# Optimization experiments

Measured on AMD Instinct MI355X. Metric: run time of the kernel, lower is better.

The kernel has to match this reference:

```python
import jax, jax.numpy as jnp
import numpy as np
import math

DIMS = 128
S = 2                     # scalar_attention_num
VS = 0.25                 # voxel_size
QS = 0.01                 # quant_size
L = int((2 * VS + 0.0001) // QS)   # 50, quant table length
GRID = int(2 / VS)        # 8
G = GRID ** 3             # 512 voxel groups
K = 32                    # points per voxel (regularized)
B = 2
N = G * K                 # 16384 points per cloud


def setup_inputs() -> dict:
    key = jax.random.key(0)
    ks = jax.random.split(key, 12)
    inputs = jax.random.normal(ks[0], (B, N, DIMS), jnp.float32)
    # coordinates scaled so per-voxel pairwise distances lie in (-VS, VS)
    coordinates = jax.random.uniform(ks[1], (B, N, 3), jnp.float32) * VS
    # groups: partition of the N points into G voxels of K points each
    groups = jnp.tile(jnp.arange(N, dtype=jnp.int32).reshape(1, G, K), (B, 1, 1))
    effective_groups = jnp.tile(jnp.arange(G, dtype=jnp.int32)[None], (B, 1))
    qkv_w = jax.random.normal(ks[2], (S, DIMS, 3 * DIMS), jnp.float32) * 0.02
    qkv_b = jnp.zeros((S, 3 * DIMS), jnp.float32)
    table_x = jax.random.normal(ks[3], (S, 3, L, DIMS), jnp.float32) * 0.02
    table_y = jax.random.normal(ks[4], (S, 3, L, DIMS), jnp.float32) * 0.02
    table_z = jax.random.normal(ks[5], (S, 3, L, DIMS), jnp.float32) * 0.02
    trans_w = jax.random.normal(ks[6], (DIMS * (S + 1), DIMS), jnp.float32) * 0.02
    trans_b = jnp.zeros((DIMS,), jnp.float32)
    ln_g = jnp.ones((DIMS,), jnp.float32)
    ln_b = jnp.zeros((DIMS,), jnp.float32)
    return {"inputs": inputs, "coordinates": coordinates, "qkv_w": qkv_w,
            "qkv_b": qkv_b, "table_x": table_x, "table_y": table_y,
            "table_z": table_z, "trans_w": trans_w, "trans_b": trans_b,
            "ln_g": ln_g, "ln_b": ln_b, "groups": groups,
            "effective_groups": effective_groups}


def reference(inputs, coordinates, qkv_w, qkv_b, table_x, table_y, table_z,
              trans_w, trans_b, ln_g, ln_b, groups, effective_groups):
    B_, N_, d = inputs.shape
    # gather points per voxel: [B,G,K,d] / [B,G,K,3]
    gflat = groups.reshape(B_, -1)
    feats = jnp.take_along_axis(inputs, gflat[..., None], axis=1).reshape(B_, G, K, d)
    coords = jnp.take_along_axis(coordinates, gflat[..., None], axis=1).reshape(B_, G, K, 3)
    # pairwise distances within each voxel: [B,G,K,K,3]
    dist = coords[:, :, :, None, :] - coords[:, :, None, :, :]
    idx = jnp.clip(jnp.floor((dist + VS) / QS).astype(jnp.int32), 0, L - 1)
    f = feats
    x = feats
    for s in range(S):
        qkv = f @ qkv_w[s] + qkv_b[s]                  # [B,G,K,3d]
        q, k, v = jnp.split(qkv, 3, axis=-1)
        enc = (table_x[s, 1][idx[..., 0]]
               + table_y[s, 1][idx[..., 1]]
               + table_z[s, 1][idx[..., 2]])           # [B,G,K,K,d]
        bias = jnp.einsum('bgid,bgijd->bgij', k, enc)
        scores = (jnp.einsum('bgid,bgjd->bgij', q, k) + bias) / math.sqrt(d)
        attn = jax.nn.softmax(scores, axis=-1)
        f = jnp.einsum('bgij,bgjd->bgid', attn, v)
        x = jnp.concatenate([x, f], axis=-1)
    # trans: Linear -> LayerNorm -> ReLU, then max-pool over points
    h = x @ trans_w + trans_b
    mu = jnp.mean(h, axis=-1, keepdims=True)
    var = jnp.var(h, axis=-1, keepdims=True)
    h = (h - mu) / jnp.sqrt(var + 1e-5) * ln_g + ln_b
    h = jax.nn.relu(h)
    pooled = jnp.max(h, axis=2)                        # [B,G,d]
    # group index i = m*GRID^2 + n*GRID + t ; output grid at [t,n,m]
    grid = pooled.reshape(B_, GRID, GRID, GRID, d).transpose(0, 3, 2, 1, 4)
    out = grid.reshape(B_, -1, d)                      # [B, GRID^3, d]
    # per-point retrieve buffer: scatter pooled feature back to each point
    for_ret = jnp.zeros((B_, N_, d), inputs.dtype)
    b_idx = jnp.arange(B_)[:, None, None]
    for_ret = for_ret.at[b_idx, groups].set(
        jnp.broadcast_to(pooled[:, :, None, :], (B_, G, K, d)))
    return out, for_ret
```

## Files before the change

kernel.cpp:

```cpp
#include <hip/hip_runtime.h>
#include <cstddef>


#define D_   128
#define VSF  0.25f
#define QSF  0.01f
#define LQ   50
#define G_   512
#define KP   32
#define BB   2
#define NP   16384
#define MT   32768
#define SCALE 0.08838834764831845f
#define NT_ALL 34
#define FRAG_S (NT_ALL * 4 * 64 * 8)

using short8 = __attribute__((ext_vector_type(8))) short;
using f32x4  = __attribute__((ext_vector_type(4))) float;

__device__ inline unsigned short f2bf(float x) {
  unsigned u = __builtin_bit_cast(unsigned, x);
  u += 0x7fffu + ((u >> 16) & 1u);
  return (unsigned short)(u >> 16);
}
__device__ inline float bu(unsigned short h) {
  return __builtin_bit_cast(float, (unsigned)h << 16);
}
__device__ inline short8 as_short8(uint4 v) {
  union { uint4 u; short8 s; } x; x.u = v; return x.s;
}

__global__ __launch_bounds__(256) void prep_tt(
    const float* __restrict__ tbl_x, const float* __restrict__ tbl_y,
    const float* __restrict__ tbl_z, float* __restrict__ Tt)
{
  const int c = threadIdx.x;
  const int s = blockIdx.x >> 7;
  const int e = blockIdx.x & 127;
  float v = 0.f;
  if (c < 150) {
    const int axis = c / 50, l = c - axis * 50;
    const float* tb = (axis == 0 ? tbl_x : (axis == 1 ? tbl_y : tbl_z));
    v = tb[(((size_t)s * 3 + 1) * LQ + l) * D_ + e];
  }
  Tt[((size_t)(s * 128 + e)) * 256 + c] = v;
}

__global__ __launch_bounds__(256) void wf_gemm(
    const float* __restrict__ qkv_w, const float* __restrict__ Tt,
    float* __restrict__ Wf)
{
  __shared__ __align__(16) float A_s[16][68];
  __shared__ __align__(16) float B_s[16][132];
  const int t  = threadIdx.x;
  const int s  = blockIdx.z;
  const float* A = qkv_w + (size_t)s * 128 * 384 + 128;
  const float* B = Tt + (size_t)s * 128 * 256;
  float* C       = Wf + (size_t)s * 128 * 256;
  const int m0 = blockIdx.x * 64;
  const int n0 = blockIdx.y * 128;
  const int r  = t >> 2;
  const int kq = (t & 3) * 4;
  const float* arow = A + (size_t)(m0 + r) * 384;
  const int kkb = t >> 4;
  const int cb  = (t & 15) * 8;
  const float* wbase = B + (size_t)kkb * 256 + n0 + cb;
  const int tx = t & 31, ty = t >> 5;

  float acc[8][4];
  #pragma unroll
  for (int i = 0; i < 8; i++)
    #pragma unroll
    for (int j = 0; j < 4; j++) acc[i][j] = 0.f;

  for (int k0 = 0; k0 < 128; k0 += 16) {
    float4 av = *(const float4*)(arow + k0 + kq);
    float4 b0 = *(const float4*)(wbase + (size_t)k0 * 256);
    float4 b1 = *(const float4*)(wbase + (size_t)k0 * 256 + 4);
    __syncthreads();
    A_s[kq + 0][r] = av.x;
    A_s[kq + 1][r] = av.y;
    A_s[kq + 2][r] = av.z;
    A_s[kq + 3][r] = av.w;
    *(float4*)&B_s[kkb][cb]     = b0;
    *(float4*)&B_s[kkb][cb + 4] = b1;
    __syncthreads();
    #pragma unroll
    for (int kk = 0; kk < 16; kk++) {
      float4 a03 = *(const float4*)&A_s[kk][ty * 8];
      float4 a47 = *(const float4*)&A_s[kk][ty * 8 + 4];
      float4 bv  = *(const float4*)&B_s[kk][tx * 4];
      float a[8] = {a03.x, a03.y, a03.z, a03.w, a47.x, a47.y, a47.z, a47.w};
      float bj[4] = {bv.x, bv.y, bv.z, bv.w};
      #pragma unroll
      for (int i = 0; i < 8; i++)
        #pragma unroll
        for (int j = 0; j < 4; j++)
          acc[i][j] += a[i] * bj[j];
    }
  }
  #pragma unroll
  for (int i = 0; i < 8; i++) {
    float4 o = {acc[i][0], acc[i][1], acc[i][2], acc[i][3]};
    *(float4*)(C + (size_t)(m0 + ty * 8 + i) * 256 + n0 + tx * 4) = o;
  }
}

__global__ __launch_bounds__(64) void pack2(
    const float* __restrict__ qkv_w, const float* __restrict__ Wf,
    const float* __restrict__ trans_w, const float* __restrict__ qkv_b,
    const float* __restrict__ Tt,
    unsigned short* __restrict__ allfrag,
    unsigned short* __restrict__ transfrag,
    float* __restrict__ bc)
{
  const int blk = blockIdx.x;
  const int lane = threadIdx.x;
  const float* B; int ldb, dstidx; unsigned short* dst; int kbase, n;
  if (blk < 192) {
    const int s = blk / 96, r = blk - s * 96;
    const int nt = r >> 2, ks = r & 3;
    B = qkv_w + (size_t)s * 128 * 384; ldb = 384;
    n = nt * 16 + (lane & 15);
    kbase = ks * 32 + ((lane >> 4) * 8);
    dst = allfrag + (size_t)s * FRAG_S;
    dstidx = nt * 4 + ks;
  } else if (blk < 272) {
    const int s = (blk - 192) / 40, r = (blk - 192) - s * 40;
    const int snt = r >> 2, ks = r & 3;
    B = Wf + (size_t)s * 32768; ldb = 256;
    n = snt * 16 + (lane & 15);
    kbase = ks * 32 + ((lane >> 4) * 8);
    dst = allfrag + (size_t)s * FRAG_S;
    dstidx = (24 + snt) * 4 + ks;
  } else if (blk < 368) {
    const int r = blk - 272;
    const int nt = r / 12, ks = r - nt * 12;
    B = trans_w; ldb = 128;
    n = nt * 16 + (lane & 15);
    kbase = ks * 32 + ((lane >> 4) * 8);
    dst = transfrag;
    dstidx = nt * 12 + ks;
  } else {
    const int s = blk - 368;
    for (int c = lane; c < 544; c += 64) {
      float v;
      if (c < 384) {
        v = qkv_b[s * 384 + c];
      } else {
        const float* bk = qkv_b + (size_t)s * 384 + 128;
        const float* T  = Tt + (size_t)s * 128 * 256 + (c - 384);
        float a = 0.f;
        #pragma unroll 4
        for (int e = 0; e < 128; e++) a += bk[e] * T[(size_t)e * 256];
        v = a;
      }
      bc[s * 544 + c] = v;
    }
    return;
  }
  unsigned v[4];
  #pragma unroll
  for (int h = 0; h < 4; h++) {
    const float x0 = B[(size_t)(kbase + 2 * h) * ldb + n];
    const float x1 = B[(size_t)(kbase + 2 * h + 1) * ldb + n];
    v[h] = f2bf(x0) | ((unsigned)f2bf(x1) << 16);
  }
  uint4 o = {v[0], v[1], v[2], v[3]};
  *(uint4*)(dst + ((size_t)dstidx * 64 + lane) * 8) = o;
}

__global__ __launch_bounds__(512, 2) void mega(
    const float* __restrict__ inputs,
    const float* __restrict__ coords,
    const int*   __restrict__ groups,
    const unsigned short* __restrict__ allfrag,
    const float* __restrict__ bc,
    const unsigned short* __restrict__ transfrag,
    const float* __restrict__ trans_b, const float* __restrict__ ln_g,
    const float* __restrict__ ln_b,
    float* __restrict__ out_all)
{
  __shared__ __align__(16) unsigned short feats_s[32][136];
  __shared__ __align__(16) unsigned short qk_s[32][424];
  __shared__ __align__(16) unsigned short vT_s[128][40];
  __shared__ __align__(16) float sc_s[32 * 33];
  __shared__ float cs[32][4];
  float (*red_s)[2][16][2] = (float (*)[2][16][2])sc_s;
  float (*wmax_s)[128]     = (float (*)[128])(sc_s + 512);
  float* pooled_s = sc_s;

  const int t   = threadIdx.x;
  const int bid = blockIdx.x;
  const int b   = bid >> 9;
  const int g   = bid & 511;
  const int wv = t >> 6, lane = t & 63, quad = lane >> 4, col = lane & 15;

  {
    const int p = t >> 4, sg = t & 15;
    const int pid = groups[(b << 14) + g * KP + p];
    const float* src = inputs + ((size_t)(b << 14) + (size_t)pid) * D_ + sg * 8;
    float4 a0 = *(const float4*)(src);
    float4 a1 = *(const float4*)(src + 4);
    uint4 o0;
    o0.x = f2bf(a0.x) | ((unsigned)f2bf(a0.y) << 16);
    o0.y = f2bf(a0.z) | ((unsigned)f2bf(a0.w) << 16);
    o0.z = f2bf(a1.x) | ((unsigned)f2bf(a1.y) << 16);
    o0.w = f2bf(a1.z) | ((unsigned)f2bf(a1.w) << 16);
    *(uint4*)&feats_s[p][sg * 8] = o0;
  }
  if (t < 32) {
    const int pid = groups[(b << 14) + g * KP + t];
    const float* cp = coords + ((size_t)(b << 14) + (size_t)pid) * 3;
    cs[t][0] = cp[0]; cs[t][1] = cp[1]; cs[t][2] = cp[2];
  }
  __syncthreads();

  const int startsA[8] = {0, 5, 10, 14, 18, 22, 26, 30};
  const int cntsA[8]   = {5, 5, 4, 4, 4, 4, 4, 4};
  const int start = startsA[wv];
  const int cnt   = cntsA[wv];

  f32x4 tacc[2];
  tacc[0] = (f32x4){0.f, 0.f, 0.f, 0.f};
  tacc[1] = (f32x4){0.f, 0.f, 0.f, 0.f};
  const uint4* tf = (const uint4*)transfrag + lane;

  for (int layer = 0; layer < 2; layer++) {
    const uint4* fr = (const uint4*)(allfrag + (size_t)layer * FRAG_S) + lane;
    const float* bcl = bc + layer * 544;

    uint4 avu[2][4];
    #pragma unroll
    for (int ks = 0; ks < 4; ks++) {
      avu[0][ks] = *(const uint4*)&feats_s[col][ks * 32 + quad * 8];
      avu[1][ks] = *(const uint4*)&feats_s[16 + col][ks * 32 + quad * 8];
    }

    uint4 bvc[4];
    #pragma unroll
    for (int ks = 0; ks < 4; ks++) bvc[ks] = fr[(start * 4 + ks) * 64];

    for (int u = 0; u < cnt; u++) {
      const int ntn = start + ((u + 1 < cnt) ? (u + 1) : u);
      uint4 bvn[4];
      #pragma unroll
      for (int ks = 0; ks < 4; ks++) bvn[ks] = fr[(ntn * 4 + ks) * 64];

      f32x4 a0 = (f32x4){0.f, 0.f, 0.f, 0.f};
      f32x4 a1 = (f32x4){0.f, 0.f, 0.f, 0.f};
      #pragma unroll
      for (int ks = 0; ks < 4; ks++) {
        short8 bv = as_short8(bvc[ks]);
        a0 = __builtin_amdgcn_mfma_f32_16x16x32_bf16(as_short8(avu[0][ks]), bv, a0, 0, 0, 0);
        a1 = __builtin_amdgcn_mfma_f32_16x16x32_bf16(as_short8(avu[1][ks]), bv, a1, 0, 0, 0);
      }
      const int nt = start + u;
      const int cc = nt * 16 + col;
      const float bsv = bcl[cc];
      if (cc >= 256 && cc < 384) {
        const unsigned lo0 = f2bf(a0[0] + bsv) | ((unsigned)f2bf(a0[1] + bsv) << 16);
        const unsigned hi0 = f2bf(a0[2] + bsv) | ((unsigned)f2bf(a0[3] + bsv) << 16);
        uint2 w0 = {lo0, hi0};
        *(uint2*)&vT_s[cc - 256][quad * 4] = w0;
        const unsigned lo1 = f2bf(a1[0] + bsv) | ((unsigned)f2bf(a1[1] + bsv) << 16);
        const unsigned hi1 = f2bf(a1[2] + bsv) | ((unsigned)f2bf(a1[3] + bsv) << 16);
        uint2 w1 = {lo1, hi1};
        *(uint2*)&vT_s[cc - 256][16 + quad * 4] = w1;
      } else {
        const int ccol = (cc < 256) ? cc : cc - 128;
        #pragma unroll
        for (int reg = 0; reg < 4; reg++) {
          qk_s[quad * 4 + reg][ccol]      = f2bf(a0[reg] + bsv);
          qk_s[16 + quad * 4 + reg][ccol] = f2bf(a1[reg] + bsv);
        }
      }
      #pragma unroll
      for (int ks = 0; ks < 4; ks++) bvc[ks] = bvn[ks];
    }
    uint4 tgv[4];
    #pragma unroll
    for (int ks = 0; ks < 4; ks++) tgv[ks] = tf[(wv * 12 + layer * 4 + ks) * 64];
    __syncthreads();

    if (wv < 4) {
      const int ihalf = wv >> 1, jhalf = wv & 1;
      f32x4 sacc = {0.f, 0.f, 0.f, 0.f};
      #pragma unroll
      for (int ks = 0; ks < 4; ks++) {
        short8 qv = as_short8(*(const uint4*)&qk_s[ihalf * 16 + col][ks * 32 + quad * 8]);
        short8 kv = as_short8(*(const uint4*)&qk_s[jhalf * 16 + col][128 + ks * 32 + quad * 8]);
        sacc = __builtin_amdgcn_mfma_f32_16x16x32_bf16(qv, kv, sacc, 0, 0, 0);
      }
      const int j = jhalf * 16 + col;
      const float cjx = cs[j][0], cjy = cs[j][1], cjz = cs[j][2];
      #pragma unroll
      for (int reg = 0; reg < 4; reg++) {
        const int i = ihalf * 16 + quad * 4 + reg;
        const float dx = cs[i][0] - cjx;
        const float dy = cs[i][1] - cjy;
        const float dz = cs[i][2] - cjz;
        int ix = (int)floorf((dx + VSF) / QSF);
        int iy = (int)floorf((dy + VSF) / QSF);
        int iz = (int)floorf((dz + VSF) / QSF);
        ix = ix < 0 ? 0 : (ix > 49 ? 49 : ix);
        iy = iy < 0 ? 0 : (iy > 49 ? 49 : iy);
        iz = iz < 0 ? 0 : (iz > 49 ? 49 : iz);
        const unsigned short* dki = &qk_s[i][256];
        const float biasv = bu(dki[ix]) + bu(dki[50 + iy]) + bu(dki[100 + iz]);
        sc_s[i * 33 + j] = (sacc[reg] + biasv) * SCALE;
      }
    }
    #pragma unroll
    for (int ks = 0; ks < 4; ks++) {
      short8 bv = as_short8(tgv[ks]);
      tacc[0] = __builtin_amdgcn_mfma_f32_16x16x32_bf16(as_short8(avu[0][ks]), bv, tacc[0], 0, 0, 0);
      tacc[1] = __builtin_amdgcn_mfma_f32_16x16x32_bf16(as_short8(avu[1][ks]), bv, tacc[1], 0, 0, 0);
    }
    __syncthreads();

    if (t < 256) {
      const int p = t >> 3, sg = t & 7;
      float vals[4];
      float lm = -1e30f;
      #pragma unroll
      for (int u = 0; u < 4; u++) {
        vals[u] = sc_s[p * 33 + sg + u * 8];
        lm = fmaxf(lm, vals[u]);
      }
      lm = fmaxf(lm, __shfl_xor(lm, 1));
      lm = fmaxf(lm, __shfl_xor(lm, 2));
      lm = fmaxf(lm, __shfl_xor(lm, 4));
      float ls = 0.f;
      #pragma unroll
      for (int u = 0; u < 4; u++) { vals[u] = __expf(vals[u] - lm); ls += vals[u]; }
      ls += __shfl_xor(ls, 1);
      ls += __shfl_xor(ls, 2);
      ls += __shfl_xor(ls, 4);
      const float inv = 1.f / ls;
      #pragma unroll
      for (int u = 0; u < 4; u++)
        qk_s[p][128 + sg + u * 8] = f2bf(vals[u] * inv);
    }
    __syncthreads();

    {
      const int mt = wv & 1, ftb = (wv >> 1) * 2;
      unsigned short* dst_base = (layer == 0) ? &feats_s[0][0] : &qk_s[0][0];
      const int dst_ld = (layer == 0) ? 136 : 424;
      short8 pv = as_short8(*(const uint4*)&qk_s[mt * 16 + col][128 + quad * 8]);
      #pragma unroll
      for (int u = 0; u < 2; u++) {
        const int ft = ftb + u;
        short8 vv = as_short8(*(const uint4*)&vT_s[ft * 16 + col][quad * 8]);
        f32x4 o = (f32x4){0.f, 0.f, 0.f, 0.f};
        o = __builtin_amdgcn_mfma_f32_16x16x32_bf16(pv, vv, o, 0, 0, 0);
        const int f = ft * 16 + col;
        #pragma unroll
        for (int reg = 0; reg < 4; reg++) {
          const int i = mt * 16 + quad * 4 + reg;
          dst_base[i * dst_ld + f] = f2bf(o[reg]);
        }
      }
    }
    __syncthreads();
  }

  const int nt = wv;
  {
    uint4 gv[4];
    #pragma unroll
    for (int ks = 0; ks < 4; ks++) gv[ks] = tf[(nt * 12 + 8 + ks) * 64];
    #pragma unroll
    for (int ks = 0; ks < 4; ks++) {
      short8 bv = as_short8(gv[ks]);
      #pragma unroll
      for (int mt = 0; mt < 2; mt++) {
        short8 av = as_short8(*(const uint4*)&qk_s[mt * 16 + col][ks * 32 + quad * 8]);
        tacc[mt] = __builtin_amdgcn_mfma_f32_16x16x32_bf16(av, bv, tacc[mt], 0, 0, 0);
      }
    }
  }
  const int c = nt * 16 + col;
  const float bsv = trans_b[c], gg = ln_g[c], lb = ln_b[c];
  float s[2][4], ssq[2][4];
  #pragma unroll
  for (int mt = 0; mt < 2; mt++)
    #pragma unroll
    for (int reg = 0; reg < 4; reg++) {
      const float v = tacc[mt][reg] + bsv;
      tacc[mt][reg] = v;
      s[mt][reg] = v; ssq[mt][reg] = v * v;
    }
  #pragma unroll
  for (int mk = 1; mk <= 8; mk <<= 1) {
    #pragma unroll
    for (int mt = 0; mt < 2; mt++)
      #pragma unroll
      for (int reg = 0; reg < 4; reg++) {
        s[mt][reg]   += __shfl_xor(s[mt][reg],   mk);
        ssq[mt][reg] += __shfl_xor(ssq[mt][reg], mk);
      }
  }
  if (col == 0) {
    #pragma unroll
    for (int mt = 0; mt < 2; mt++)
      #pragma unroll
      for (int reg = 0; reg < 4; reg++) {
        red_s[wv][mt][quad * 4 + reg][0] = s[mt][reg];
        red_s[wv][mt][quad * 4 + reg][1] = ssq[mt][reg];
      }
  }
  __syncthreads();
  float mu[2][4], rstd[2][4];
  #pragma unroll
  for (int mt = 0; mt < 2; mt++)
    #pragma unroll
    for (int reg = 0; reg < 4; reg++) {
      float st = 0.f, sst = 0.f;
      #pragma unroll
      for (int w = 0; w < 8; w++) {
        st  += red_s[w][mt][quad * 4 + reg][0];
        sst += red_s[w][mt][quad * 4 + reg][1];
      }
      mu[mt][reg] = st * (1.f / 128.f);
      const float var = sst * (1.f / 128.f) - mu[mt][reg] * mu[mt][reg];
      rstd[mt][reg] = rsqrtf(var + 1e-5f);
    }
  float cm[2];
  #pragma unroll
  for (int mt = 0; mt < 2; mt++) {
    float mx = 0.f;
    #pragma unroll
    for (int reg = 0; reg < 4; reg++) {
      float v = (tacc[mt][reg] - mu[mt][reg]) * rstd[mt][reg] * gg + lb;
      v = fmaxf(v, 0.f);
      mx = fmaxf(mx, v);
    }
    cm[mt] = mx;
  }
  #pragma unroll
  for (int mt = 0; mt < 2; mt++) {
    cm[mt] = fmaxf(cm[mt], __shfl_xor(cm[mt], 16));
    cm[mt] = fmaxf(cm[mt], __shfl_xor(cm[mt], 32));
  }
  __syncthreads();
  if (quad == 0) {
    #pragma unroll
    for (int mt = 0; mt < 2; mt++)
      wmax_s[mt][c] = cm[mt];
  }
  __syncthreads();

  if (t < 128) {
    const int cc = t;
    const float mx = fmaxf(wmax_s[0][cc], wmax_s[1][cc]);
    pooled_s[cc] = mx;
    const int mm = g >> 6, nn = (g >> 3) & 7, tt2 = g & 7;
    const int opos = tt2 * 64 + nn * 8 + mm;
    out_all[((size_t)b * G_ + opos) * D_ + cc] = mx;
  }
  __syncthreads();

  if (t < 256) {
    const int p = t >> 3, sg = t & 7;
    const int pid = groups[(b << 14) + g * KP + p];
    float* dst = out_all + (size_t)BB * G_ * D_
               + ((size_t)(b << 14) + (size_t)pid) * D_ + sg * 16;
    #pragma unroll
    for (int u = 0; u < 4; u++)
      *(float4*)(dst + u * 4) = *(const float4*)&pooled_s[sg * 16 + u * 4];
  }
}

extern "C" void kernel_launch(void* const* d_in, const int* in_sizes, int n_in,
                              void* d_out, int out_size, void* d_ws, size_t ws_size,
                              hipStream_t stream) {
  const float* inputs  = (const float*)d_in[0];
  const float* coords  = (const float*)d_in[1];
  const float* qkv_w   = (const float*)d_in[2];
  const float* qkv_b   = (const float*)d_in[3];
  const float* tbl_x   = (const float*)d_in[4];
  const float* tbl_y   = (const float*)d_in[5];
  const float* tbl_z   = (const float*)d_in[6];
  const float* trans_w = (const float*)d_in[7];
  const float* trans_b = (const float*)d_in[8];
  const float* ln_g    = (const float*)d_in[9];
  const float* ln_b    = (const float*)d_in[10];
  const int*   groups  = (const int*)d_in[11];

  float* out = (float*)d_out;
  unsigned short* allfrag   = (unsigned short*)d_ws;
  unsigned short* transfrag = allfrag + 2 * FRAG_S;
  float* Tt  = (float*)(transfrag + 96 * 512);
  float* Wf  = Tt + (size_t)2 * 128 * 256;
  float* bc  = Wf + (size_t)2 * 128 * 256;

  prep_tt<<<256, 256, 0, stream>>>(tbl_x, tbl_y, tbl_z, Tt);
  wf_gemm<<<dim3(2, 2, 2), 256, 0, stream>>>(qkv_w, Tt, Wf);
  pack2<<<370, 64, 0, stream>>>(qkv_w, Wf, trans_w, qkv_b, Tt,
                                allfrag, transfrag, bc);

  mega<<<BB * G_, 512, 0, stream>>>(inputs, coords, groups, allfrag, bc,
                                    transfrag, trans_b, ln_g, ln_b, out);
}
```

Baseline: 165.5 us.

## Fuse table-transpose, Wf GEMM and fragment packing into one prep kernel

Replaces the three preprocessing kernels (table transpose, small fp32 GEMM producing Wf, and bf16 fragment packing) with a single prep_all kernel. The blocks that pack the Wf fragments now compute their 32x16 tile of the Wk·T product directly from LDS-staged weights and table rows, and the bias-column block dots against the table rows directly. This removes two kernel launches and the Tt/Wf workspace round trips, at the cost of some redundant loads of weight rows across the fragment blocks.

```diff
diff --git a/kernel.cpp b/kernel.cpp
--- a/kernel.cpp
+++ b/kernel.cpp
@@ -30,92 +30,92 @@
   union { uint4 u; short8 s; } x; x.u = v; return x.s;
 }
 
-__global__ __launch_bounds__(256) void prep_tt(
+__global__ __launch_bounds__(64) void prep_all(
+    const float* __restrict__ qkv_w, const float* __restrict__ trans_w,
+    const float* __restrict__ qkv_b,
     const float* __restrict__ tbl_x, const float* __restrict__ tbl_y,
-    const float* __restrict__ tbl_z, float* __restrict__ Tt)
-{
-  const int c = threadIdx.x;
-  const int s = blockIdx.x >> 7;
-  const int e = blockIdx.x & 127;
-  float v = 0.f;
-  if (c < 150) {
-    const int axis = c / 50, l = c - axis * 50;
-    const float* tb = (axis == 0 ? tbl_x : (axis == 1 ? tbl_y : tbl_z));
-    v = tb[(((size_t)s * 3 + 1) * LQ + l) * D_ + e];
-  }
-  Tt[((size_t)(s * 128 + e)) * 256 + c] = v;
-}
-
-__global__ __launch_bounds__(256) void wf_gemm(
-    const float* __restrict__ qkv_w, const float* __restrict__ Tt,
-    float* __restrict__ Wf)
-{
-  __shared__ __align__(16) float A_s[16][68];
-  __shared__ __align__(16) float B_s[16][132];
-  const int t  = threadIdx.x;
-  const int s  = blockIdx.z;
-  const float* A = qkv_w + (size_t)s * 128 * 384 + 128;
-  const float* B = Tt + (size_t)s * 128 * 256;
-  float* C       = Wf + (size_t)s * 128 * 256;
-  const int m0 = blockIdx.x * 64;
-  const int n0 = blockIdx.y * 128;
-  const int r  = t >> 2;
-  const int kq = (t & 3) * 4;
-  const float* arow = A + (size_t)(m0 + r) * 384;
-  const int kkb = t >> 4;
-  const int cb  = (t & 15) * 8;
-  const float* wbase = B + (size_t)kkb * 256 + n0 + cb;
-  const int tx = t & 31, ty = t >> 5;
-
-  float acc[8][4];
-  #pragma unroll
-  for (int i = 0; i < 8; i++)
-    #pragma unroll
-    for (int j = 0; j < 4; j++) acc[i][j] = 0.f;
-
-  for (int k0 = 0; k0 < 128; k0 += 16) {
-    float4 av = *(const float4*)(arow + k0 + kq);
-    float4 b0 = *(const float4*)(wbase + (size_t)k0 * 256);
-    float4 b1 = *(const float4*)(wbase + (size_t)k0 * 256 + 4);
-    __syncthreads();
-    A_s[kq + 0][r] = av.x;
-    A_s[kq + 1][r] = av.y;
-    A_s[kq + 2][r] = av.z;
-    A_s[kq + 3][r] = av.w;
-    *(float4*)&B_s[kkb][cb]     = b0;
-    *(float4*)&B_s[kkb][cb + 4] = b1;
-    __syncthreads();
-    #pragma unroll
-    for (int kk = 0; kk < 16; kk++) {
-      float4 a03 = *(const float4*)&A_s[kk][ty * 8];
-      float4 a47 = *(const float4*)&A_s[kk][ty * 8 + 4];
-      float4 bv  = *(const float4*)&B_s[kk][tx * 4];
-      float a[8] = {a03.x, a03.y, a03.z, a03.w, a47.x, a47.y, a47.z, a47.w};
-      float bj[4] = {bv.x, bv.y, bv.z, bv.w};
-      #pragma unroll
-      for (int i = 0; i < 8; i++)
-        #pragma unroll
-        for (int j = 0; j < 4; j++)
-          acc[i][j] += a[i] * bj[j];
-    }
-  }
-  #pragma unroll
-  for (int i = 0; i < 8; i++) {
-    float4 o = {acc[i][0], acc[i][1], acc[i][2], acc[i][3]};
-    *(float4*)(C + (size_t)(m0 + ty * 8 + i) * 256 + n0 + tx * 4) = o;
-  }
-}
-
-__global__ __launch_bounds__(64) void pack2(
-    const float* __restrict__ qkv_w, const float* __restrict__ Wf,
-    const float* __restrict__ trans_w, const float* __restrict__ qkv_b,
-    const float* __restrict__ Tt,
+    const float* __restrict__ tbl_z,
     unsigned short* __restrict__ allfrag,
     unsigned short* __restrict__ transfrag,
     float* __restrict__ bc)
 {
-  const int blk = blockIdx.x;
+  __shared__ __align__(16) float As[32][132];
+  __shared__ __align__(16) float Ts[16][132];
+
+  const int blk  = blockIdx.x;
   const int lane = threadIdx.x;
+
+  if (blk >= 192 && blk < 272) {
+    const int s = (blk - 192) / 40, r = (blk - 192) - s * 40;
+    const int snt = r >> 2, ks = r & 3;
+    const float* Abase = qkv_w + (size_t)s * 128 * 384 + 128;
+    for (int i = lane; i < 32 * 32; i += 64) {
+      const int m = i >> 5, q = i & 31;
+      float4 v = *(const float4*)(Abase + (size_t)(ks * 32 + m) * 384 + q * 4);
+      *(float4*)&As[m][q * 4] = v;
+    }
+    for (int i = lane; i < 16 * 32; i += 64) {
+      const int cl = i >> 5, q = i & 31;
+      const int c = snt * 16 + cl;
+      float4 v = {0.f, 0.f, 0.f, 0.f};
+      if (c < 150) {
+        const int axis = c / 50, l = c - axis * 50;
+        const float* tb = (axis == 0 ? tbl_x : (axis == 1 ? tbl_y : tbl_z));
+        v = *(const float4*)(tb + (((size_t)s * 3 + 1) * LQ + l) * D_ + q * 4);
+      }
+      *(float4*)&Ts[cl][q * 4] = v;
+    }
+    __syncthreads();
+    const int cl = lane & 15, mb = (lane >> 4) * 8;
+    float acc[8];
+    #pragma unroll
+    for (int m = 0; m < 8; m++) acc[m] = 0.f;
+    for (int e = 0; e < 128; e += 4) {
+      float4 tv = *(const float4*)&Ts[cl][e];
+      #pragma unroll
+      for (int m = 0; m < 8; m++) {
+        float4 av = *(const float4*)&As[mb + m][e];
+        acc[m] += av.x * tv.x;
+        acc[m] += av.y * tv.y;
+        acc[m] += av.z * tv.z;
+        acc[m] += av.w * tv.w;
+      }
+    }
+    unsigned v[4];
+    #pragma unroll
+    for (int h = 0; h < 4; h++)
+      v[h] = f2bf(acc[2 * h]) | ((unsigned)f2bf(acc[2 * h + 1]) << 16);
+    uint4 o = {v[0], v[1], v[2], v[3]};
+    unsigned short* dst = allfrag + (size_t)s * FRAG_S;
+    const int dstidx = (24 + snt) * 4 + ks;
+    *(uint4*)(dst + ((size_t)dstidx * 64 + lane) * 8) = o;
+    return;
+  }
+
+  if (blk >= 368) {
+    const int s = blk - 368;
+    for (int c = lane; c < 544; c += 64) {
+      float v;
+      if (c < 384) {
+        v = qkv_b[s * 384 + c];
+      } else {
+        const int cc = c - 384;
+        float a = 0.f;
+        if (cc < 150) {
+          const int axis = cc / 50, l = cc - axis * 50;
+          const float* tb = (axis == 0 ? tbl_x : (axis == 1 ? tbl_y : tbl_z));
+          const float* tr = tb + (((size_t)s * 3 + 1) * LQ + l) * D_;
+          const float* bk = qkv_b + (size_t)s * 384 + 128;
+          #pragma unroll 4
+          for (int e = 0; e < 128; e++) a += bk[e] * tr[e];
+        }
+        v = a;
+      }
+      bc[s * 544 + c] = v;
+    }
+    return;
+  }
+
   const float* B; int ldb, dstidx; unsigned short* dst; int kbase, n;
   if (blk < 192) {
     const int s = blk / 96, r = blk - s * 96;
@@ -125,15 +125,7 @@
     kbase = ks * 32 + ((lane >> 4) * 8);
     dst = allfrag + (size_t)s * FRAG_S;
     dstidx = nt * 4 + ks;
-  } else if (blk < 272) {
-    const int s = (blk - 192) / 40, r = (blk - 192) - s * 40;
-    const int snt = r >> 2, ks = r & 3;
-    B = Wf + (size_t)s * 32768; ldb = 256;
-    n = snt * 16 + (lane & 15);
-    kbase = ks * 32 + ((lane >> 4) * 8);
-    dst = allfrag + (size_t)s * FRAG_S;
-    dstidx = (24 + snt) * 4 + ks;
-  } else if (blk < 368) {
+  } else {
     const int r = blk - 272;
     const int nt = r / 12, ks = r - nt * 12;
     B = trans_w; ldb = 128;
@@ -141,23 +133,6 @@
     kbase = ks * 32 + ((lane >> 4) * 8);
     dst = transfrag;
     dstidx = nt * 12 + ks;
-  } else {
-    const int s = blk - 368;
-    for (int c = lane; c < 544; c += 64) {
-      float v;
-      if (c < 384) {
-        v = qkv_b[s * 384 + c];
-      } else {
-        const float* bk = qkv_b + (size_t)s * 384 + 128;
-        const float* T  = Tt + (size_t)s * 128 * 256 + (c - 384);
-        float a = 0.f;
-        #pragma unroll 4
-        for (int e = 0; e < 128; e++) a += bk[e] * T[(size_t)e * 256];
-        v = a;
-      }
-      bc[s * 544 + c] = v;
-    }
-    return;
   }
   unsigned v[4];
   #pragma unroll
@@ -492,14 +467,11 @@
   float* out = (float*)d_out;
   unsigned short* allfrag   = (unsigned short*)d_ws;
   unsigned short* transfrag = allfrag + 2 * FRAG_S;
-  float* Tt  = (float*)(transfrag + 96 * 512);
-  float* Wf  = Tt + (size_t)2 * 128 * 256;
-  float* bc  = Wf + (size_t)2 * 128 * 256;
-
-  prep_tt<<<256, 256, 0, stream>>>(tbl_x, tbl_y, tbl_z, Tt);
-  wf_gemm<<<dim3(2, 2, 2), 256, 0, stream>>>(qkv_w, Tt, Wf);
-  pack2<<<370, 64, 0, stream>>>(qkv_w, Wf, trans_w, qkv_b, Tt,
-                                allfrag, transfrag, bc);
+  float* bc  = (float*)(transfrag + 96 * 512);
+
+  prep_all<<<370, 64, 0, stream>>>(qkv_w, trans_w, qkv_b,
+                                   tbl_x, tbl_y, tbl_z,
+                                   allfrag, transfrag, bc);
 
   mega<<<BB * G_, 512, 0, stream>>>(inputs, coords, groups, allfrag, bc,
                                     transfrag, trans_b, ln_g, ln_b, out);
```

After: 140.2 us, median of 2. 1.18x faster.
